# Kernel optimization log

Hardware: AMD Instinct MI355X
Metric: run time of the kernel (lower is better)

## Reference

```python
import jax, jax.numpy as jnp
import numpy as np

NUM_SEQS = 16
NUM_HEADS = 32
NUM_KV_HEADS = 8
HEAD_SIZE = 128
BLOCK_SIZE = 16
X = 8  # vectorized key-cache packing factor
MAX_CTX = 4096
MAX_BLOCKS = MAX_CTX // BLOCK_SIZE
NUM_BLOCKS = NUM_SEQS * MAX_BLOCKS
SCALE = 0.08838834764831845  # 1/sqrt(128)
NEG_INF = -1e30


def setup_inputs() -> dict:
    key0 = jax.random.key(0)
    ks = jax.random.split(key0, 5)
    query = jax.random.normal(ks[0], (NUM_SEQS, 1, NUM_HEADS * HEAD_SIZE), jnp.float32)
    key = jax.random.normal(ks[1], (NUM_SEQS, 1, NUM_KV_HEADS * HEAD_SIZE), jnp.float32)
    value = jax.random.normal(ks[2], (NUM_SEQS, 1, NUM_KV_HEADS * HEAD_SIZE), jnp.float32)
    key_cache = jax.random.normal(ks[3], (NUM_BLOCKS, NUM_KV_HEADS, HEAD_SIZE // X, BLOCK_SIZE, X), jnp.float32)
    value_cache = jax.random.normal(ks[4], (NUM_BLOCKS, NUM_KV_HEADS, HEAD_SIZE, BLOCK_SIZE), jnp.float32)
    rng = np.random.default_rng(0)
    block_tables = rng.permutation(NUM_BLOCKS).reshape(NUM_SEQS, MAX_BLOCKS).astype(np.int32)
    context_lens = rng.integers(256, MAX_CTX + 1, size=(NUM_SEQS,)).astype(np.int32)
    last = context_lens - 1
    slots = block_tables[np.arange(NUM_SEQS), last // BLOCK_SIZE].astype(np.int64) * BLOCK_SIZE + (last % BLOCK_SIZE)
    slot_mapping = slots.reshape(NUM_SEQS, 1)
    return {
        'query': query, 'key': key, 'value': value,
        'key_cache': key_cache, 'value_cache': value_cache,
        'block_tables': jnp.asarray(block_tables),
        'context_lens': jnp.asarray(context_lens),
        'slot_mapping': jnp.asarray(slot_mapping),
    }


def _paged_attention_decode(query, key, value, key_cache, value_cache, block_tables, context_lens, slot_mapping):
    S, L1, hidden = query.shape  # L1 == 1 (decode)
    nb, kvH, _, bs, x = key_cache.shape
    D = value_cache.shape[2]
    H = hidden // D
    G = H // kvH  # queries per kv head
    maxB = block_tables.shape[1]

    q = query.reshape(S, H, D)
    k_new = key.reshape(S, kvH, D)
    v_new = value.reshape(S, kvH, D)

    # --- reshape_and_cache: write new K/V into paged caches ---
    sm = slot_mapping.reshape(-1)
    blk, off = sm // bs, sm % bs
    key_cache = key_cache.at[blk, :, :, off, :].set(k_new.reshape(S, kvH, D // x, x))
    value_cache = value_cache.at[blk, :, :, off].set(v_new)

    # --- gather paged KV via block tables ---
    # key_cache [nb,kvH,D/x,bs,x] -> [nb,kvH,bs,D]
    kc = key_cache.transpose(0, 1, 3, 2, 4).reshape(nb, kvH, bs, D)
    vc = value_cache.transpose(0, 1, 3, 2)  # [nb,kvH,bs,D]
    keys = kc[block_tables].transpose(0, 1, 3, 2, 4).reshape(S, maxB * bs, kvH, D)
    vals = vc[block_tables].transpose(0, 1, 3, 2, 4).reshape(S, maxB * bs, kvH, D)

    # --- GQA attention with context-length masking ---
    qg = q.reshape(S, kvH, G, D)
    scores = jnp.einsum('skgd,slkd->skgl', qg, keys) * jnp.asarray(SCALE, q.dtype)
    valid = jnp.arange(maxB * bs)[None, :] < context_lens[:, None]  # [S,L]
    scores = jnp.where(valid[:, None, None, :], scores, NEG_INF)
    probs = jax.nn.softmax(scores, axis=-1)
    out = jnp.einsum('skgl,slkd->skgd', probs, vals)
    return out.reshape(S, 1, H * D)


def reference(query, key, value, key_cache, value_cache, block_tables, context_lens, slot_mapping):
    return _paged_attention_decode(query, key, value, key_cache, value_cache,
                                   block_tables, context_lens, slot_mapping)
```

## Files before the change

### kernel.cpp

```cpp
#include <hip/hip_runtime.h>

#define NSEQ   16
#define KVH    8
#define NG     4
#define HD     128
#define BS     16
#define MAXB   256
#define PART   256
#define NPART  16
#define WPT    64
#define PSTRIDE 520
#define SCALE_F 0.08838834764831845f

__global__ __launch_bounds__(256) void pa_partial_kernel(
    const float* __restrict__ query,
    const float* __restrict__ key,
    const float* __restrict__ value,
    const float* __restrict__ key_cache,
    const float* __restrict__ value_cache,
    const int*   __restrict__ block_tables,
    const int*   __restrict__ context_lens,
    float*       __restrict__ ws)
{
    const int bid = blockIdx.x;
    const int p   = bid & (NPART - 1);
    const int kvh = (bid >> 4) & (KVH - 1);
    const int s   = bid >> 7;

    const int ctx = context_lens[s];
    const int t0  = p * PART;
    if (t0 >= ctx) return;

    __shared__ float p_lds[4][NG][WPT];
    __shared__ float o_lds[4][NG * HD];
    __shared__ float ml_lds[4][8];

    const int tid  = threadIdx.x;
    const int wv   = tid >> 6;
    const int lane = tid & 63;
    const int tw0  = t0 + wv * WPT;
    const bool wact = (tw0 < ctx);

    const float* q = query + (size_t)s * (KVH * NG * HD) + (size_t)kvh * (NG * HD);

    float m_w = -1e30f;
    float l_w[NG] = {0.f, 0.f, 0.f, 0.f};

    if (wact) {
        const int t  = tw0 + lane;
        const int bt = block_tables[s * MAXB + (t >> 4)];
        const float* kb = key_cache + (size_t)bt * (KVH * HD * BS)
                                    + (size_t)kvh * (HD * BS) + (t & 15) * 8;

        float sc[NG] = {0.f, 0.f, 0.f, 0.f};
        #pragma unroll
        for (int j = 0; j < 16; ++j) {
            const float4 ka = *(const float4*)(kb + j * 128);
            const float4 kc = *(const float4*)(kb + j * 128 + 4);
            #pragma unroll
            for (int g = 0; g < NG; ++g) {
                sc[g] += q[g * HD + j * 8 + 0] * ka.x + q[g * HD + j * 8 + 1] * ka.y
                       + q[g * HD + j * 8 + 2] * ka.z + q[g * HD + j * 8 + 3] * ka.w
                       + q[g * HD + j * 8 + 4] * kc.x + q[g * HD + j * 8 + 5] * kc.y
                       + q[g * HD + j * 8 + 6] * kc.z + q[g * HD + j * 8 + 7] * kc.w;
            }
        }

        if (t == ctx - 1) {
            const float4* kn4 = (const float4*)(key + ((size_t)s * KVH + kvh) * HD);
            float ns[NG] = {0.f, 0.f, 0.f, 0.f};
            #pragma unroll
            for (int c = 0; c < 32; ++c) {
                const float4 k4 = kn4[c];
                #pragma unroll
                for (int g = 0; g < NG; ++g) {
                    ns[g] += q[g * HD + c * 4 + 0] * k4.x + q[g * HD + c * 4 + 1] * k4.y
                           + q[g * HD + c * 4 + 2] * k4.z + q[g * HD + c * 4 + 3] * k4.w;
                }
            }
            #pragma unroll
            for (int g = 0; g < NG; ++g) sc[g] = ns[g];
        }

        float mv;
        if (t < ctx) {
            #pragma unroll
            for (int g = 0; g < NG; ++g) sc[g] *= SCALE_F;
            mv = fmaxf(fmaxf(sc[0], sc[1]), fmaxf(sc[2], sc[3]));
        } else {
            #pragma unroll
            for (int g = 0; g < NG; ++g) sc[g] = -1e30f;
            mv = -1e30f;
        }

        #pragma unroll
        for (int o = 32; o; o >>= 1) mv = fmaxf(mv, __shfl_xor(mv, o));
        m_w = mv;

        float pr[NG];
        #pragma unroll
        for (int g = 0; g < NG; ++g) {
            pr[g] = __expf(sc[g] - m_w);
            p_lds[wv][g][lane] = pr[g];
            l_w[g] = pr[g];
        }
        #pragma unroll
        for (int o = 32; o; o >>= 1) {
            l_w[0] += __shfl_xor(l_w[0], o);
            l_w[1] += __shfl_xor(l_w[1], o);
            l_w[2] += __shfl_xor(l_w[2], o);
            l_w[3] += __shfl_xor(l_w[3], o);
        }
    }

    if (lane == 0) {
        ml_lds[wv][0] = m_w;
        #pragma unroll
        for (int g = 0; g < NG; ++g) ml_lds[wv][1 + g] = l_w[g];
    }

    if (wact) {
        const int nbv = min(4, (ctx - tw0 + 15) >> 4);
        int btv[4];
        #pragma unroll
        for (int b = 0; b < 4; ++b)
            btv[b] = block_tables[s * MAXB + (tw0 >> 4) + b];

        const int tl = ctx - 1 - tw0;
        const float4* pl4 = (const float4*)&p_lds[wv][0][0];

        #pragma unroll 2
        for (int half = 0; half < 2; ++half) {
            const int d = lane + half * 64;
            float a[NG] = {0.f, 0.f, 0.f, 0.f};
            for (int b = 0; b < nbv; ++b) {
                const float* vb = value_cache + (size_t)btv[b] * (KVH * HD * BS)
                                              + (size_t)kvh * (HD * BS) + d * BS;
                #pragma unroll
                for (int c = 0; c < 4; ++c) {
                    const float4 v4 = *(const float4*)(vb + c * 4);
                    #pragma unroll
                    for (int g = 0; g < NG; ++g) {
                        const float4 pg = pl4[g * 16 + b * 4 + c];
                        a[g] += pg.x * v4.x + pg.y * v4.y + pg.z * v4.z + pg.w * v4.w;
                    }
                }
            }
            if (tl >= 0 && tl < WPT) {
                const int btn = block_tables[s * MAXB + ((ctx - 1) >> 4)];
                const float vold = value_cache[(size_t)btn * (KVH * HD * BS)
                                               + (size_t)kvh * (HD * BS) + d * BS + ((ctx - 1) & 15)];
                const float vnew = value[((size_t)s * KVH + kvh) * HD + d];
                const float dv = vnew - vold;
                #pragma unroll
                for (int g = 0; g < NG; ++g) a[g] += p_lds[wv][g][tl] * dv;
            }
            #pragma unroll
            for (int g = 0; g < NG; ++g) o_lds[wv][g * HD + d] = a[g];
        }
    } else {
        #pragma unroll
        for (int i = 0; i < 8; ++i) o_lds[wv][i * 64 + lane] = 0.f;
    }

    __syncthreads();

    const float m0 = ml_lds[0][0], m1 = ml_lds[1][0], m2 = ml_lds[2][0], m3 = ml_lds[3][0];
    const float M  = fmaxf(fmaxf(m0, m1), fmaxf(m2, m3));
    const float w0 = __expf(m0 - M), w1 = __expf(m1 - M);
    const float w2 = __expf(m2 - M), w3 = __expf(m3 - M);

    float* rec = ws + (size_t)bid * PSTRIDE;
    #pragma unroll
    for (int r = 0; r < 2; ++r) {
        const int idx = tid + r * 256;
        rec[idx] = w0 * o_lds[0][idx] + w1 * o_lds[1][idx]
                 + w2 * o_lds[2][idx] + w3 * o_lds[3][idx];
    }
    if (tid < NG) {
        rec[512 + tid] = w0 * ml_lds[0][1 + tid] + w1 * ml_lds[1][1 + tid]
                       + w2 * ml_lds[2][1 + tid] + w3 * ml_lds[3][1 + tid];
    }
    if (tid == 4) rec[516] = M;
}

__global__ __launch_bounds__(128) void pa_reduce_kernel(
    const float* __restrict__ ws,
    const int*   __restrict__ context_lens,
    float*       __restrict__ out)
{
    const int b    = blockIdx.x;
    const int g    = b & 3;
    const int pair = b >> 2;
    const int s    = pair >> 3;
    const int kvh  = pair & 7;
    const int ctx  = context_lens[s];
    const int np   = (ctx + PART - 1) / PART;

    const int d = threadIdx.x;
    const float* base = ws + (size_t)pair * NPART * PSTRIDE;

    float M = -1e30f;
    for (int p2 = 0; p2 < np; ++p2) M = fmaxf(M, base[p2 * PSTRIDE + 516]);

    float L = 0.f, acc = 0.f;
    for (int p2 = 0; p2 < np; ++p2) {
        const float* rec = base + p2 * PSTRIDE;
        const float w = __expf(rec[516] - M);
        L   += w * rec[512 + g];
        acc += w * rec[g * HD + d];
    }

    out[(size_t)s * (KVH * NG * HD) + (size_t)(kvh * NG + g) * HD + d] = acc / L;
}

extern "C" void kernel_launch(void* const* d_in, const int* in_sizes, int n_in,
                              void* d_out, int out_size, void* d_ws, size_t ws_size,
                              hipStream_t stream) {
    const float* query       = (const float*)d_in[0];
    const float* key         = (const float*)d_in[1];
    const float* value       = (const float*)d_in[2];
    const float* key_cache   = (const float*)d_in[3];
    const float* value_cache = (const float*)d_in[4];
    const int*   block_tables  = (const int*)d_in[5];
    const int*   context_lens  = (const int*)d_in[6];

    float* out = (float*)d_out;
    float* ws  = (float*)d_ws;

    pa_partial_kernel<<<NSEQ * KVH * NPART, 256, 0, stream>>>(
        query, key, value, key_cache, value_cache, block_tables, context_lens, ws);
    pa_reduce_kernel<<<NSEQ * KVH * NG, 128, 0, stream>>>(ws, context_lens, out);
}
```

Baseline: 85.93 us.

## Prefetch K and V tiles into registers before softmax and stage query in LDS

Each wave now loads all of its key vectors and both halves of its value tile into registers up front. The value loads are issued before the softmax reductions, so their memory latency overlaps with the score computation. The query slice is staged once in shared memory and read as float4, and launch bounds request at least 3 blocks per CU. The cost is much higher register pressure (about 256 floats of prefetch per lane), which risks spills or lower occupancy. Value loads are also issued for all four blocks regardless of the context length, adding some traffic on tail partitions.

```diff
diff --git a/kernel.cpp b/kernel.cpp
--- a/kernel.cpp
+++ b/kernel.cpp
@@ -12,7 +12,7 @@
 #define PSTRIDE 520
 #define SCALE_F 0.08838834764831845f
 
-__global__ __launch_bounds__(256) void pa_partial_kernel(
+__global__ __launch_bounds__(256, 3) void pa_partial_kernel(
     const float* __restrict__ query,
     const float* __restrict__ key,
     const float* __restrict__ value,
@@ -31,6 +31,7 @@
     const int t0  = p * PART;
     if (t0 >= ctx) return;
 
+    __shared__ float q_lds[NG * HD];
     __shared__ float p_lds[4][NG][WPT];
     __shared__ float o_lds[4][NG * HD];
     __shared__ float ml_lds[4][8];
@@ -41,7 +42,9 @@
     const int tw0  = t0 + wv * WPT;
     const bool wact = (tw0 < ctx);
 
-    const float* q = query + (size_t)s * (KVH * NG * HD) + (size_t)kvh * (NG * HD);
+    const float* qsrc = query + ((size_t)s * KVH + kvh) * (NG * HD);
+    ((float2*)q_lds)[tid] = ((const float2*)qsrc)[tid];
+    __syncthreads();
 
     float m_w = -1e30f;
     float l_w[NG] = {0.f, 0.f, 0.f, 0.f};
@@ -52,17 +55,24 @@
         const float* kb = key_cache + (size_t)bt * (KVH * HD * BS)
                                     + (size_t)kvh * (HD * BS) + (t & 15) * 8;
 
+        float4 kr[32];
+        #pragma unroll
+        for (int j = 0; j < 16; ++j) {
+            kr[2 * j]     = *(const float4*)(kb + j * 128);
+            kr[2 * j + 1] = *(const float4*)(kb + j * 128 + 4);
+        }
+
         float sc[NG] = {0.f, 0.f, 0.f, 0.f};
         #pragma unroll
         for (int j = 0; j < 16; ++j) {
-            const float4 ka = *(const float4*)(kb + j * 128);
-            const float4 kc = *(const float4*)(kb + j * 128 + 4);
+            const float4 ka = kr[2 * j];
+            const float4 kc = kr[2 * j + 1];
             #pragma unroll
             for (int g = 0; g < NG; ++g) {
-                sc[g] += q[g * HD + j * 8 + 0] * ka.x + q[g * HD + j * 8 + 1] * ka.y
-                       + q[g * HD + j * 8 + 2] * ka.z + q[g * HD + j * 8 + 3] * ka.w
-                       + q[g * HD + j * 8 + 4] * kc.x + q[g * HD + j * 8 + 5] * kc.y
-                       + q[g * HD + j * 8 + 6] * kc.z + q[g * HD + j * 8 + 7] * kc.w;
+                const float4 qa = *(const float4*)(&q_lds[g * HD + j * 8]);
+                const float4 qb = *(const float4*)(&q_lds[g * HD + j * 8 + 4]);
+                sc[g] += qa.x * ka.x + qa.y * ka.y + qa.z * ka.z + qa.w * ka.w
+                       + qb.x * kc.x + qb.y * kc.y + qb.z * kc.z + qb.w * kc.w;
             }
         }
 
@@ -74,12 +84,30 @@
                 const float4 k4 = kn4[c];
                 #pragma unroll
                 for (int g = 0; g < NG; ++g) {
-                    ns[g] += q[g * HD + c * 4 + 0] * k4.x + q[g * HD + c * 4 + 1] * k4.y
-                           + q[g * HD + c * 4 + 2] * k4.z + q[g * HD + c * 4 + 3] * k4.w;
+                    ns[g] += q_lds[g * HD + c * 4 + 0] * k4.x + q_lds[g * HD + c * 4 + 1] * k4.y
+                           + q_lds[g * HD + c * 4 + 2] * k4.z + q_lds[g * HD + c * 4 + 3] * k4.w;
                 }
             }
             #pragma unroll
             for (int g = 0; g < NG; ++g) sc[g] = ns[g];
+        }
+
+        int btv[4];
+        #pragma unroll
+        for (int b = 0; b < 4; ++b)
+            btv[b] = block_tables[s * MAXB + (tw0 >> 4) + b];
+
+        float4 vr0[16], vr1[16];
+        #pragma unroll
+        for (int b = 0; b < 4; ++b) {
+            const float* vb0 = value_cache + (size_t)btv[b] * (KVH * HD * BS)
+                                           + (size_t)kvh * (HD * BS) + lane * BS;
+            const float* vb1 = vb0 + 64 * BS;
+            #pragma unroll
+            for (int c = 0; c < 4; ++c) {
+                vr0[b * 4 + c] = *(const float4*)(vb0 + c * 4);
+                vr1[b * 4 + c] = *(const float4*)(vb1 + c * 4);
+            }
         }
 
         float mv;
@@ -92,7 +120,6 @@
             for (int g = 0; g < NG; ++g) sc[g] = -1e30f;
             mv = -1e30f;
         }
-
         #pragma unroll
         for (int o = 32; o; o >>= 1) mv = fmaxf(mv, __shfl_xor(mv, o));
         m_w = mv;
@@ -111,54 +138,57 @@
             l_w[2] += __shfl_xor(l_w[2], o);
             l_w[3] += __shfl_xor(l_w[3], o);
         }
-    }
-
-    if (lane == 0) {
-        ml_lds[wv][0] = m_w;
-        #pragma unroll
-        for (int g = 0; g < NG; ++g) ml_lds[wv][1 + g] = l_w[g];
-    }
-
-    if (wact) {
-        const int nbv = min(4, (ctx - tw0 + 15) >> 4);
-        int btv[4];
-        #pragma unroll
-        for (int b = 0; b < 4; ++b)
-            btv[b] = block_tables[s * MAXB + (tw0 >> 4) + b];
+
+        if (lane == 0) {
+            ml_lds[wv][0] = m_w;
+            #pragma unroll
+            for (int g = 0; g < NG; ++g) ml_lds[wv][1 + g] = l_w[g];
+        }
+
+        float a0[NG] = {0.f, 0.f, 0.f, 0.f};
+        float a1[NG] = {0.f, 0.f, 0.f, 0.f};
+        const float4* pl4 = (const float4*)&p_lds[wv][0][0];
+        #pragma unroll
+        for (int b = 0; b < 4; ++b) {
+            #pragma unroll
+            for (int c = 0; c < 4; ++c) {
+                const float4 v0 = vr0[b * 4 + c];
+                const float4 v1 = vr1[b * 4 + c];
+                #pragma unroll
+                for (int g = 0; g < NG; ++g) {
+                    const float4 pg = pl4[g * 16 + b * 4 + c];
+                    a0[g] += pg.x * v0.x + pg.y * v0.y + pg.z * v0.z + pg.w * v0.w;
+                    a1[g] += pg.x * v1.x + pg.y * v1.y + pg.z * v1.z + pg.w * v1.w;
+                }
+            }
+        }
 
         const int tl = ctx - 1 - tw0;
-        const float4* pl4 = (const float4*)&p_lds[wv][0][0];
-
-        #pragma unroll 2
-        for (int half = 0; half < 2; ++half) {
-            const int d = lane + half * 64;
-            float a[NG] = {0.f, 0.f, 0.f, 0.f};
-            for (int b = 0; b < nbv; ++b) {
-                const float* vb = value_cache + (size_t)btv[b] * (KVH * HD * BS)
-                                              + (size_t)kvh * (HD * BS) + d * BS;
-                #pragma unroll
-                for (int c = 0; c < 4; ++c) {
-                    const float4 v4 = *(const float4*)(vb + c * 4);
-                    #pragma unroll
-                    for (int g = 0; g < NG; ++g) {
-                        const float4 pg = pl4[g * 16 + b * 4 + c];
-                        a[g] += pg.x * v4.x + pg.y * v4.y + pg.z * v4.z + pg.w * v4.w;
-                    }
-                }
-            }
-            if (tl >= 0 && tl < WPT) {
-                const int btn = block_tables[s * MAXB + ((ctx - 1) >> 4)];
-                const float vold = value_cache[(size_t)btn * (KVH * HD * BS)
-                                               + (size_t)kvh * (HD * BS) + d * BS + ((ctx - 1) & 15)];
-                const float vnew = value[((size_t)s * KVH + kvh) * HD + d];
-                const float dv = vnew - vold;
-                #pragma unroll
-                for (int g = 0; g < NG; ++g) a[g] += p_lds[wv][g][tl] * dv;
-            }
-            #pragma unroll
-            for (int g = 0; g < NG; ++g) o_lds[wv][g * HD + d] = a[g];
+        if (tl >= 0 && tl < WPT) {
+            const int btn = block_tables[s * MAXB + ((ctx - 1) >> 4)];
+            const float* vbase = value_cache + (size_t)btn * (KVH * HD * BS)
+                                             + (size_t)kvh * (HD * BS) + ((ctx - 1) & 15);
+            const float dv0 = value[((size_t)s * KVH + kvh) * HD + lane]      - vbase[lane * BS];
+            const float dv1 = value[((size_t)s * KVH + kvh) * HD + lane + 64] - vbase[(lane + 64) * BS];
+            #pragma unroll
+            for (int g = 0; g < NG; ++g) {
+                const float pt = p_lds[wv][g][tl];
+                a0[g] += pt * dv0;
+                a1[g] += pt * dv1;
+            }
+        }
+
+        #pragma unroll
+        for (int g = 0; g < NG; ++g) {
+            o_lds[wv][g * HD + lane]      = a0[g];
+            o_lds[wv][g * HD + 64 + lane] = a1[g];
         }
     } else {
+        if (lane == 0) {
+            ml_lds[wv][0] = -1e30f;
+            #pragma unroll
+            for (int g = 0; g < NG; ++g) ml_lds[wv][1 + g] = 0.f;
+        }
         #pragma unroll
         for (int i = 0; i < 8; ++i) o_lds[wv][i * 64 + lane] = 0.f;
     }
```

After: 244.6 us. +184.6%, slower.

## Convert partial attention kernel to persistent workers with atomic work queue

Applied to the files above, without the earlier changes.

The partial kernel now launches a fixed pool of 1024 persistent blocks. Each block repeatedly grabs a work item (sequence, kv-head, partition) from a global atomic counter instead of getting one block per item. The intent is to cut block launch and early-exit overhead for the many empty partitions and to balance uneven context lengths. In exchange it adds a memset launch, an atomic plus two barriers per item, and serialised item fetching within each block.

```diff
diff --git a/kernel.cpp b/kernel.cpp
--- a/kernel.cpp
+++ b/kernel.cpp
@@ -8,9 +8,12 @@
 #define MAXB   256
 #define PART   256
 #define NPART  16
+#define NITEMS (NSEQ * KVH * NPART)
 #define WPT    64
 #define PSTRIDE 520
+#define REC_BYTES ((size_t)NITEMS * PSTRIDE * 4)
 #define SCALE_F 0.08838834764831845f
+#define NWORKERS 1024
 
 __global__ __launch_bounds__(256) void pa_partial_kernel(
     const float* __restrict__ query,
@@ -20,168 +23,177 @@
     const float* __restrict__ value_cache,
     const int*   __restrict__ block_tables,
     const int*   __restrict__ context_lens,
-    float*       __restrict__ ws)
+    float*       __restrict__ ws,
+    unsigned int* __restrict__ counter)
 {
-    const int bid = blockIdx.x;
-    const int p   = bid & (NPART - 1);
-    const int kvh = (bid >> 4) & (KVH - 1);
-    const int s   = bid >> 7;
-
-    const int ctx = context_lens[s];
-    const int t0  = p * PART;
-    if (t0 >= ctx) return;
-
     __shared__ float p_lds[4][NG][WPT];
     __shared__ float o_lds[4][NG * HD];
     __shared__ float ml_lds[4][8];
+    __shared__ int   item_s;
 
     const int tid  = threadIdx.x;
     const int wv   = tid >> 6;
     const int lane = tid & 63;
-    const int tw0  = t0 + wv * WPT;
-    const bool wact = (tw0 < ctx);
-
-    const float* q = query + (size_t)s * (KVH * NG * HD) + (size_t)kvh * (NG * HD);
-
-    float m_w = -1e30f;
-    float l_w[NG] = {0.f, 0.f, 0.f, 0.f};
-
-    if (wact) {
-        const int t  = tw0 + lane;
-        const int bt = block_tables[s * MAXB + (t >> 4)];
-        const float* kb = key_cache + (size_t)bt * (KVH * HD * BS)
-                                    + (size_t)kvh * (HD * BS) + (t & 15) * 8;
-
-        float sc[NG] = {0.f, 0.f, 0.f, 0.f};
-        #pragma unroll
-        for (int j = 0; j < 16; ++j) {
-            const float4 ka = *(const float4*)(kb + j * 128);
-            const float4 kc = *(const float4*)(kb + j * 128 + 4);
-            #pragma unroll
-            for (int g = 0; g < NG; ++g) {
-                sc[g] += q[g * HD + j * 8 + 0] * ka.x + q[g * HD + j * 8 + 1] * ka.y
-                       + q[g * HD + j * 8 + 2] * ka.z + q[g * HD + j * 8 + 3] * ka.w
-                       + q[g * HD + j * 8 + 4] * kc.x + q[g * HD + j * 8 + 5] * kc.y
-                       + q[g * HD + j * 8 + 6] * kc.z + q[g * HD + j * 8 + 7] * kc.w;
-            }
-        }
-
-        if (t == ctx - 1) {
-            const float4* kn4 = (const float4*)(key + ((size_t)s * KVH + kvh) * HD);
-            float ns[NG] = {0.f, 0.f, 0.f, 0.f};
-            #pragma unroll
-            for (int c = 0; c < 32; ++c) {
-                const float4 k4 = kn4[c];
+
+    for (;;) {
+        if (tid == 0) item_s = (int)atomicAdd(counter, 1u);
+        __syncthreads();
+        const int item = item_s;
+        __syncthreads();
+        if (item >= NITEMS) return;
+
+        const int p   = item & (NPART - 1);
+        const int kvh = (item >> 4) & (KVH - 1);
+        const int s   = item >> 7;
+        const int ctx = context_lens[s];
+        const int t0  = p * PART;
+        if (t0 >= ctx) continue;
+
+        const int tw0  = t0 + wv * WPT;
+        const bool wact = (tw0 < ctx);
+
+        const float* q = query + ((size_t)s * KVH + kvh) * (NG * HD);
+
+        float m_w = -1e30f;
+        float l_w[NG] = {0.f, 0.f, 0.f, 0.f};
+
+        if (wact) {
+            const int t  = tw0 + lane;
+            const int bt = block_tables[s * MAXB + (t >> 4)];
+            const float* kb = key_cache + (size_t)bt * (KVH * HD * BS)
+                                        + (size_t)kvh * (HD * BS) + (t & 15) * 8;
+
+            float sc[NG] = {0.f, 0.f, 0.f, 0.f};
+            #pragma unroll
+            for (int j = 0; j < 16; ++j) {
+                const float4 ka = *(const float4*)(kb + j * 128);
+                const float4 kc = *(const float4*)(kb + j * 128 + 4);
                 #pragma unroll
                 for (int g = 0; g < NG; ++g) {
-                    ns[g] += q[g * HD + c * 4 + 0] * k4.x + q[g * HD + c * 4 + 1] * k4.y
-                           + q[g * HD + c * 4 + 2] * k4.z + q[g * HD + c * 4 + 3] * k4.w;
-                }
-            }
-            #pragma unroll
-            for (int g = 0; g < NG; ++g) sc[g] = ns[g];
-        }
-
-        float mv;
-        if (t < ctx) {
-            #pragma unroll
-            for (int g = 0; g < NG; ++g) sc[g] *= SCALE_F;
-            mv = fmaxf(fmaxf(sc[0], sc[1]), fmaxf(sc[2], sc[3]));
-        } else {
-            #pragma unroll
-            for (int g = 0; g < NG; ++g) sc[g] = -1e30f;
-            mv = -1e30f;
-        }
-
-        #pragma unroll
-        for (int o = 32; o; o >>= 1) mv = fmaxf(mv, __shfl_xor(mv, o));
-        m_w = mv;
-
-        float pr[NG];
-        #pragma unroll
-        for (int g = 0; g < NG; ++g) {
-            pr[g] = __expf(sc[g] - m_w);
-            p_lds[wv][g][lane] = pr[g];
-            l_w[g] = pr[g];
-        }
-        #pragma unroll
-        for (int o = 32; o; o >>= 1) {
-            l_w[0] += __shfl_xor(l_w[0], o);
-            l_w[1] += __shfl_xor(l_w[1], o);
-            l_w[2] += __shfl_xor(l_w[2], o);
-            l_w[3] += __shfl_xor(l_w[3], o);
-        }
-    }
-
-    if (lane == 0) {
-        ml_lds[wv][0] = m_w;
-        #pragma unroll
-        for (int g = 0; g < NG; ++g) ml_lds[wv][1 + g] = l_w[g];
-    }
-
-    if (wact) {
-        const int nbv = min(4, (ctx - tw0 + 15) >> 4);
-        int btv[4];
-        #pragma unroll
-        for (int b = 0; b < 4; ++b)
-            btv[b] = block_tables[s * MAXB + (tw0 >> 4) + b];
-
-        const int tl = ctx - 1 - tw0;
-        const float4* pl4 = (const float4*)&p_lds[wv][0][0];
-
-        #pragma unroll 2
-        for (int half = 0; half < 2; ++half) {
-            const int d = lane + half * 64;
-            float a[NG] = {0.f, 0.f, 0.f, 0.f};
-            for (int b = 0; b < nbv; ++b) {
-                const float* vb = value_cache + (size_t)btv[b] * (KVH * HD * BS)
-                                              + (size_t)kvh * (HD * BS) + d * BS;
-                #pragma unroll
-                for (int c = 0; c < 4; ++c) {
-                    const float4 v4 = *(const float4*)(vb + c * 4);
+                    sc[g] += q[g * HD + j * 8 + 0] * ka.x + q[g * HD + j * 8 + 1] * ka.y
+                           + q[g * HD + j * 8 + 2] * ka.z + q[g * HD + j * 8 + 3] * ka.w
+                           + q[g * HD + j * 8 + 4] * kc.x + q[g * HD + j * 8 + 5] * kc.y
+                           + q[g * HD + j * 8 + 6] * kc.z + q[g * HD + j * 8 + 7] * kc.w;
+                }
+            }
+
+            if (t == ctx - 1) {
+                const float4* kn4 = (const float4*)(key + ((size_t)s * KVH + kvh) * HD);
+                float ns[NG] = {0.f, 0.f, 0.f, 0.f};
+                #pragma unroll
+                for (int c = 0; c < 32; ++c) {
+                    const float4 k4 = kn4[c];
                     #pragma unroll
                     for (int g = 0; g < NG; ++g) {
-                        const float4 pg = pl4[g * 16 + b * 4 + c];
-                        a[g] += pg.x * v4.x + pg.y * v4.y + pg.z * v4.z + pg.w * v4.w;
+                        ns[g] += q[g * HD + c * 4 + 0] * k4.x + q[g * HD + c * 4 + 1] * k4.y
+                               + q[g * HD + c * 4 + 2] * k4.z + q[g * HD + c * 4 + 3] * k4.w;
                     }
                 }
-            }
-            if (tl >= 0 && tl < WPT) {
-                const int btn = block_tables[s * MAXB + ((ctx - 1) >> 4)];
-                const float vold = value_cache[(size_t)btn * (KVH * HD * BS)
-                                               + (size_t)kvh * (HD * BS) + d * BS + ((ctx - 1) & 15)];
-                const float vnew = value[((size_t)s * KVH + kvh) * HD + d];
-                const float dv = vnew - vold;
-                #pragma unroll
-                for (int g = 0; g < NG; ++g) a[g] += p_lds[wv][g][tl] * dv;
-            }
-            #pragma unroll
-            for (int g = 0; g < NG; ++g) o_lds[wv][g * HD + d] = a[g];
-        }
-    } else {
+                #pragma unroll
+                for (int g = 0; g < NG; ++g) sc[g] = ns[g];
+            }
+
+            float mv;
+            if (t < ctx) {
+                #pragma unroll
+                for (int g = 0; g < NG; ++g) sc[g] *= SCALE_F;
+                mv = fmaxf(fmaxf(sc[0], sc[1]), fmaxf(sc[2], sc[3]));
+            } else {
+                #pragma unroll
+                for (int g = 0; g < NG; ++g) sc[g] = -1e30f;
+                mv = -1e30f;
+            }
+
+            #pragma unroll
+            for (int o = 32; o; o >>= 1) mv = fmaxf(mv, __shfl_xor(mv, o));
+            m_w = mv;
+
+            float pr[NG];
+            #pragma unroll
+            for (int g = 0; g < NG; ++g) {
+                pr[g] = __expf(sc[g] - m_w);
+                p_lds[wv][g][lane] = pr[g];
+                l_w[g] = pr[g];
+            }
+            #pragma unroll
+            for (int o = 32; o; o >>= 1) {
+                l_w[0] += __shfl_xor(l_w[0], o);
+                l_w[1] += __shfl_xor(l_w[1], o);
+                l_w[2] += __shfl_xor(l_w[2], o);
+                l_w[3] += __shfl_xor(l_w[3], o);
+            }
+        }
+
+        if (lane == 0) {
+            ml_lds[wv][0] = m_w;
+            #pragma unroll
+            for (int g = 0; g < NG; ++g) ml_lds[wv][1 + g] = l_w[g];
+        }
+
+        if (wact) {
+            const int nbv = min(4, (ctx - tw0 + 15) >> 4);
+            int btv[4];
+            #pragma unroll
+            for (int b = 0; b < 4; ++b)
+                btv[b] = block_tables[s * MAXB + (tw0 >> 4) + b];
+
+            const int tl = ctx - 1 - tw0;
+            const float4* pl4 = (const float4*)&p_lds[wv][0][0];
+
+            #pragma unroll 2
+            for (int half = 0; half < 2; ++half) {
+                const int d = lane + half * 64;
+                float a[NG] = {0.f, 0.f, 0.f, 0.f};
+                for (int b = 0; b < nbv; ++b) {
+                    const float* vb = value_cache + (size_t)btv[b] * (KVH * HD * BS)
+                                                  + (size_t)kvh * (HD * BS) + d * BS;
+                    #pragma unroll
+                    for (int c = 0; c < 4; ++c) {
+                        const float4 v4 = *(const float4*)(vb + c * 4);
+                        #pragma unroll
+                        for (int g = 0; g < NG; ++g) {
+                            const float4 pg = pl4[g * 16 + b * 4 + c];
+                            a[g] += pg.x * v4.x + pg.y * v4.y + pg.z * v4.z + pg.w * v4.w;
+                        }
+                    }
+                }
+                if (tl >= 0 && tl < WPT) {
+                    const int btn = block_tables[s * MAXB + ((ctx - 1) >> 4)];
+                    const float vold = value_cache[(size_t)btn * (KVH * HD * BS)
+                                                   + (size_t)kvh * (HD * BS) + d * BS + ((ctx - 1) & 15)];
+                    const float vnew = value[((size_t)s * KVH + kvh) * HD + d];
+                    const float dv = vnew - vold;
+                    #pragma unroll
+                    for (int g = 0; g < NG; ++g) a[g] += p_lds[wv][g][tl] * dv;
+                }
+                #pragma unroll
+                for (int g = 0; g < NG; ++g) o_lds[wv][g * HD + d] = a[g];
+            }
+        } else {
+            #pragma unroll
+            for (int i = 0; i < 8; ++i) o_lds[wv][i * 64 + lane] = 0.f;
+        }
+
+        __syncthreads();
+
+        const float m0 = ml_lds[0][0], m1 = ml_lds[1][0], m2 = ml_lds[2][0], m3 = ml_lds[3][0];
+        const float M  = fmaxf(fmaxf(m0, m1), fmaxf(m2, m3));
+        const float w0 = __expf(m0 - M), w1 = __expf(m1 - M);
+        const float w2 = __expf(m2 - M), w3 = __expf(m3 - M);
+
+        float* rec = ws + (size_t)item * PSTRIDE;
         #pragma unroll
-        for (int i = 0; i < 8; ++i) o_lds[wv][i * 64 + lane] = 0.f;
+        for (int r = 0; r < 2; ++r) {
+            const int idx = tid + r * 256;
+            rec[idx] = w0 * o_lds[0][idx] + w1 * o_lds[1][idx]
+                     + w2 * o_lds[2][idx] + w3 * o_lds[3][idx];
+        }
+        if (tid < NG) {
+            rec[512 + tid] = w0 * ml_lds[0][1 + tid] + w1 * ml_lds[1][1 + tid]
+                           + w2 * ml_lds[2][1 + tid] + w3 * ml_lds[3][1 + tid];
+        }
+        if (tid == 4) rec[516] = M;
     }
-
-    __syncthreads();
-
-    const float m0 = ml_lds[0][0], m1 = ml_lds[1][0], m2 = ml_lds[2][0], m3 = ml_lds[3][0];
-    const float M  = fmaxf(fmaxf(m0, m1), fmaxf(m2, m3));
-    const float w0 = __expf(m0 - M), w1 = __expf(m1 - M);
-    const float w2 = __expf(m2 - M), w3 = __expf(m3 - M);
-
-    float* rec = ws + (size_t)bid * PSTRIDE;
-    #pragma unroll
-    for (int r = 0; r < 2; ++r) {
-        const int idx = tid + r * 256;
-        rec[idx] = w0 * o_lds[0][idx] + w1 * o_lds[1][idx]
-                 + w2 * o_lds[2][idx] + w3 * o_lds[3][idx];
-    }
-    if (tid < NG) {
-        rec[512 + tid] = w0 * ml_lds[0][1 + tid] + w1 * ml_lds[1][1 + tid]
-                       + w2 * ml_lds[2][1 + tid] + w3 * ml_lds[3][1 + tid];
-    }
-    if (tid == 4) rec[516] = M;
 }
 
 __global__ __launch_bounds__(128) void pa_reduce_kernel(
@@ -227,8 +239,10 @@
 
     float* out = (float*)d_out;
     float* ws  = (float*)d_ws;
-
-    pa_partial_kernel<<<NSEQ * KVH * NPART, 256, 0, stream>>>(
-        query, key, value, key_cache, value_cache, block_tables, context_lens, ws);
+    unsigned int* counter = (unsigned int*)((char*)d_ws + REC_BYTES);
+
+    hipMemsetAsync(counter, 0, sizeof(unsigned int), stream);
+    pa_partial_kernel<<<NWORKERS, 256, 0, stream>>>(
+        query, key, value, key_cache, value_cache, block_tables, context_lens, ws, counter);
     pa_reduce_kernel<<<NSEQ * KVH * NG, 128, 0, stream>>>(ws, context_lens, out);
 }
```

New measurement: 85.02 us. Within noise of the previous version (-1.1%).
